# Optimization experiments

Measured on AMD Instinct MI355X. Metric: run time of the kernel, lower is better.

The kernel has to match this reference:

```python
import jax, jax.numpy as jnp
import numpy as np

GRID_SIZE = 16
KH = KW = 3


def setup_inputs() -> dict:
    key = jax.random.key(0)
    k1, k2, k3, k4 = jax.random.split(key, 4)
    B, H, W, C, F = 8, 32, 32, 64, 64
    x = jax.random.normal(k1, (B, H, W, C), dtype=jnp.float32)
    control_points = jax.random.normal(k2, (F, C, KH, KW, GRID_SIZE), dtype=jnp.float32) * 0.1
    w1 = jax.random.normal(k3, (F, C, KH, KW), dtype=jnp.float32) * 0.1
    w2 = jax.random.normal(k4, (F, C, KH, KW), dtype=jnp.float32) * 0.1
    return {"x": x, "control_points": control_points, "w1": w1, "w2": w2}


def _extract_patches_same(x, kh, kw):
    # x: (B,H,W,C), stride 1, TF 'SAME' padding -> (B,H,W,kh,kw,C)
    B, H, W, C = x.shape
    ph, pw = kh - 1, kw - 1
    xp = jnp.pad(x, ((0, 0), (ph // 2, ph - ph // 2), (pw // 2, pw - pw // 2), (0, 0)))
    taps = [xp[:, i:i + H, j:j + W, :] for i in range(kh) for j in range(kw)]
    return jnp.stack(taps, axis=3).reshape(B, H, W, kh, kw, C)


def reference(x, control_points, w1, w2):
    F, C, kh, kw, G = control_points.shape
    grid = jnp.linspace(-1.0, 1.0, G)
    patches = _extract_patches_same(x, kh, kw)  # (B,H,W,kh,kw,C)
    # spline: searchsorted + clip + linear interp on the fixed uniform grid
    xc = jnp.clip(patches, -1.0, 1.0)
    idx = jnp.clip(jnp.searchsorted(grid, xc, side='left') - 1, 0, G - 2)
    frac = (xc - grid[idx]) / (grid[idx + 1] - grid[idx])  # (B,H,W,kh,kw,C)
    # two-nonzero linear basis over control points -> (B,H,W,kh,kw,C,G)
    basis = (jax.nn.one_hot(idx, G, dtype=x.dtype) * (1.0 - frac)[..., None]
             + jax.nn.one_hot(idx + 1, G, dtype=x.dtype) * frac[..., None])
    # fuse w1 into control points, contract taps+channels+grid in one einsum
    wcp = w1[..., None] * control_points  # (F,C,kh,kw,G)
    out = jnp.einsum('bpqijcg,fcijg->bpqf', basis, wcp)
    out = out + jnp.einsum('bpqijc,fcij->bpqf', jax.nn.silu(patches), w2)
    return out  # (B,H,W,F)
```

## Files before the change

kernel.cpp:

```cpp
#include <hip/hip_runtime.h>


typedef _Float16 v8h __attribute__((ext_vector_type(8)));
typedef float    v4f __attribute__((ext_vector_type(4)));

#define NSLOT8  81920
#define NOUT4   131072

__global__ __launch_bounds__(256) void prep_wsw(const float* __restrict__ cp,
                                                const float* __restrict__ w1,
                                                const float* __restrict__ w2,
                                                _Float16* __restrict__ wsw,
                                                float* __restrict__ out) {
    int tid = blockIdx.x * 256 + threadIdx.x;
    if (tid < NSLOT8) {
        int lane = tid & 63;
        int rest = tid >> 6;
        int nt   = rest & 3;
        int ks   = rest >> 2;
        int kb   = ks * 32 + ((lane >> 4) << 3);
        int f    = (nt << 4) + (lane & 15);
        int chunk = kb / 640;
        int klb   = kb - chunk * 640;
        v8h o;
        if (klb < 576) {
            int c  = (chunk << 2) + klb / 144;
            int rb = klb % 144;
            int ij = rb >> 4;
            float w = w1[f * 576 + c * 9 + ij];
            const v4f* cpp = (const v4f*)(cp + (size_t)f * 9216 + c * 144 + rb);
            v4f lo = cpp[0], hi = cpp[1];
#pragma unroll
            for (int j = 0; j < 4; ++j) {
            o[j]     = (_Float16)(w * lo[j]);
            o[j + 4] = (_Float16)(w * hi[j]);
            }
        } else {
            int i2 = klb - 576;
            int c  = (chunk << 2) + (i2 >> 4);
            if ((i2 & 15) == 0) {
#pragma unroll
                for (int j = 0; j < 8; ++j)
                    o[j] = (_Float16)w2[f * 576 + c * 9 + j];
            } else {
#pragma unroll
                for (int j = 0; j < 8; ++j) o[j] = (_Float16)0.f;
                o[0] = (_Float16)w2[f * 576 + c * 9 + 8];
            }
        }
        ((v8h*)wsw)[tid] = o;
    }
    if (tid < NOUT4) ((v4f*)out)[tid] = (v4f){0.f, 0.f, 0.f, 0.f};
}

__global__ __launch_bounds__(256, 3) void kan_mfma(const float* __restrict__ x,
                                                   const _Float16* __restrict__ wsw,
                                                   float* __restrict__ out) {
    __shared__ __align__(16) char smem[41472];
    _Float16* sb  = (_Float16*)smem;
    float*    red = (float*)smem;

    int blk   = blockIdx.x;
    int kh    = blk >> 8;
    int rowid = blk & 255;
    int b = rowid >> 5, p = rowid & 31;
    int t = threadIdx.x, wv = t >> 6, lane = t & 63;
    int m = lane & 15, kq = lane >> 4;

    const int chs[4] = {0, 6, 11, 16};
    int ch0 = chs[kh], ch1 = chs[kh + 1];

    const float* xb = x + (size_t)b * 65536;

    int xoff[2], sbb[2], silb[2];
    unsigned prevPack[2] = {0u, 0u};
#pragma unroll
    for (int it = 0; it < 2; ++it) {
        int e  = t + it * 256;
        int ec = e < 288 ? e : 0;
        int px = ec / 9;
        int ij = ec - px * 9;
        int di = ij / 3;
        int dj = ij - di * 3;
        int row = p + di - 1;
        int col = px + dj - 1;
        bool ok  = ((unsigned)row < 32u) && ((unsigned)col < 32u);
        xoff[it] = ok ? ((row * 32 + col) * 64) : -1;
        sbb[it]  = px * 648 + ij * 16;
        silb[it] = px * 648 + 576 + ij;
    }

    v4f z4 = (v4f){0.f, 0.f, 0.f, 0.f};

    v4f vbuf[2];
#pragma unroll
    for (int it = 0; it < 2; ++it)
        vbuf[it] = (xoff[it] >= 0) ? *(const v4f*)(xb + xoff[it] + ch0 * 4) : z4;

    for (int i4 = t; i4 < 2592; i4 += 256) ((v4f*)sb)[i4] = z4;

    v4f acc[2][4];
#pragma unroll
    for (int i = 0; i < 2; ++i)
#pragma unroll
        for (int n = 0; n < 4; ++n) acc[i][n] = z4;

    __syncthreads();

    for (int gch = ch0; gch < ch1; ++gch) {
#pragma unroll
        for (int it = 0; it < 2; ++it) {
            if (t + it * 256 < 288) {
                v4f xv = vbuf[it];
                unsigned pp = prevPack[it];
                unsigned np = 0;
                _Float16* rp = sb + sbb[it];
                _Float16* sp = sb + silb[it];
#pragma unroll
                for (int cl = 0; cl < 4; ++cl) {
                    float v  = xv[cl];
                    float xc = fminf(fmaxf(v, -1.f), 1.f);
                    float tt = (xc + 1.f) * 7.5f;
                    int idx  = (int)tt;
                    if (idx > 14) idx = 14;
                    float fr = tt - (float)idx;
                    float sv = v * __builtin_amdgcn_rcpf(1.f + __expf(-v));
                    _Float16* q = rp + cl * 144;
                    if (gch > ch0) {
                        int pi = (pp >> (cl * 8)) & 255;
                        q[pi]     = (_Float16)0.f;
                        q[pi + 1] = (_Float16)0.f;
                    }
                    q[idx]     = (_Float16)(1.f - fr);
                    q[idx + 1] = (_Float16)fr;
                    sp[cl * 16] = (_Float16)sv;
                    np |= (unsigned)idx << (cl * 8);
                }
                prevPack[it] = np;
            }
        }
        __syncthreads();
        if (gch + 1 < ch1) {
#pragma unroll
            for (int it = 0; it < 2; ++it)
                vbuf[it] = (xoff[it] >= 0)
                         ? *(const v4f*)(xb + xoff[it] + (gch + 1) * 4) : z4;
        }
        const _Float16* ap = sb + m * 648 + (wv * 5) * 32 + kq * 8;
        const v8h* bp = (const v8h*)wsw + ((size_t)gch * 20 + wv * 5) * 256 + lane;
        v8h a0c = *(const v8h*)ap;
        v8h a1c = *(const v8h*)(ap + 16 * 648);
        v8h b0c = bp[0], b1c = bp[64], b2c = bp[128], b3c = bp[192];
#pragma unroll
        for (int s = 0; s < 5; ++s) {
            v8h a0n, a1n, b0n, b1n, b2n, b3n;
            if (s < 4) {
                const _Float16* ap2 = ap + (s + 1) * 32;
                a0n = *(const v8h*)ap2;
                a1n = *(const v8h*)(ap2 + 16 * 648);
                const v8h* bp2 = bp + (s + 1) * 256;
                b0n = bp2[0];
                b1n = bp2[64];
                b2n = bp2[128];
                b3n = bp2[192];
            }
            acc[0][0] = __builtin_amdgcn_mfma_f32_16x16x32_f16(a0c, b0c, acc[0][0], 0, 0, 0);
            acc[0][1] = __builtin_amdgcn_mfma_f32_16x16x32_f16(a0c, b1c, acc[0][1], 0, 0, 0);
            acc[0][2] = __builtin_amdgcn_mfma_f32_16x16x32_f16(a0c, b2c, acc[0][2], 0, 0, 0);
            acc[0][3] = __builtin_amdgcn_mfma_f32_16x16x32_f16(a0c, b3c, acc[0][3], 0, 0, 0);
            acc[1][0] = __builtin_amdgcn_mfma_f32_16x16x32_f16(a1c, b0c, acc[1][0], 0, 0, 0);
            acc[1][1] = __builtin_amdgcn_mfma_f32_16x16x32_f16(a1c, b1c, acc[1][1], 0, 0, 0);
            acc[1][2] = __builtin_amdgcn_mfma_f32_16x16x32_f16(a1c, b2c, acc[1][2], 0, 0, 0);
            acc[1][3] = __builtin_amdgcn_mfma_f32_16x16x32_f16(a1c, b3c, acc[1][3], 0, 0, 0);
            if (s < 4) {
                a0c = a0n; a1c = a1n;
                b0c = b0n; b1c = b1n; b2c = b2n; b3c = b3n;
            }
        }
        __syncthreads();
    }

#pragma unroll
    for (int mt = 0; mt < 2; ++mt)
#pragma unroll
        for (int nt = 0; nt < 4; ++nt)
#pragma unroll
            for (int r = 0; r < 4; ++r)
                red[wv * 2080 + (mt * 16 + kq * 4 + r) * 65 + nt * 16 + m] = acc[mt][nt][r];
    __syncthreads();
    int f = t & 63, pxg = t >> 6;
    float* op = out + (size_t)rowid * 2048 + f;
#pragma unroll
    for (int i = 0; i < 8; ++i) {
        int px = pxg * 8 + i;
        float s = red[px * 65 + f] + red[2080 + px * 65 + f]
                + red[4160 + px * 65 + f] + red[6240 + px * 65 + f];
        atomicAdd(op + px * 64, s);
    }
}

extern "C" void kernel_launch(void* const* d_in, const int* in_sizes, int n_in,
                              void* d_out, int out_size, void* d_ws, size_t ws_size,
                              hipStream_t stream) {
    const float* x  = (const float*)d_in[0];
    const float* cp = (const float*)d_in[1];
    const float* w1 = (const float*)d_in[2];
    const float* w2 = (const float*)d_in[3];
    _Float16* wsw = (_Float16*)d_ws;
    float*    outp = (float*)d_out;

    prep_wsw<<<512, 256, 0, stream>>>(cp, w1, w2, wsw, outp);
    kan_mfma<<<768, 256, 0, stream>>>(x, wsw, outp);
}
```

Measured before the change: 87.84 us.

## Build spline and SiLU MFMA A-fragments in registers instead of via LDS

Each lane now builds its own A-operand fragment straight from global x. Spline fragments come from clamp/index math on one value per row, placing the two nonzero basis weights. SiLU fragments gather up to eight neighbouring taps. This removes the shared-memory basis buffer, its zero-fill and scatter stores, and the two barriers per channel group. In exchange it reloads x redundantly across lanes and waves, recomputes exp for SiLU taps, and drops the explicit software prefetch of A and B fragments.

```diff
diff --git a/kernel.cpp b/kernel.cpp
--- a/kernel.cpp
+++ b/kernel.cpp
@@ -3,6 +3,8 @@
 
 typedef _Float16 v8h __attribute__((ext_vector_type(8)));
 typedef float    v4f __attribute__((ext_vector_type(4)));
+typedef unsigned int u32;
+typedef u32      v4u __attribute__((ext_vector_type(4)));
 
 #define NSLOT8  81920
 #define NOUT4   131072
@@ -32,8 +34,8 @@
             v4f lo = cpp[0], hi = cpp[1];
 #pragma unroll
             for (int j = 0; j < 4; ++j) {
-            o[j]     = (_Float16)(w * lo[j]);
-            o[j + 4] = (_Float16)(w * hi[j]);
+                o[j]     = (_Float16)(w * lo[j]);
+                o[j + 4] = (_Float16)(w * hi[j]);
             }
         } else {
             int i2 = klb - 576;
@@ -53,12 +55,61 @@
     if (tid < NOUT4) ((v4f*)out)[tid] = (v4f){0.f, 0.f, 0.f, 0.f};
 }
 
+__device__ inline u32 h2u(float f) {
+    union { _Float16 h; unsigned short u; } c;
+    c.h = (_Float16)f;
+    return (u32)c.u;
+}
+
+__device__ inline v8h spline_frag(float v, int g0) {
+    float xc = fminf(fmaxf(v, -1.f), 1.f);
+    float tt = (xc + 1.f) * 7.5f;
+    int idx  = (int)tt;
+    if (idx > 14) idx = 14;
+    float fr = tt - (float)idx;
+    int r0 = idx - g0;
+    u32 lo = h2u(1.f - fr);
+    u32 hi = h2u(fr);
+    u32 pair = lo | (hi << 16);
+    int wq = r0 >> 1;
+    int ro = r0 & 1;
+    v4u w;
+#pragma unroll
+    for (int q = 0; q < 4; ++q) {
+        u32 val = (q == wq) ? (ro ? (lo << 16) : pair)
+                            : ((ro && q == wq + 1) ? hi : 0u);
+        w[q] = val;
+    }
+    union { v4u u; v8h h; } cvt;
+    cvt.u = w;
+    return cvt.h;
+}
+
+__device__ inline v8h silu_frag(const float* __restrict__ xb, int xc,
+                                int p, int pxq, int ijh) {
+    v8h a;
+#pragma unroll
+    for (int j = 0; j < 8; ++j) {
+        int ij = ijh + j;
+        float sv = 0.f;
+        if (ij < 9) {
+            int di = (ij * 11) >> 5;
+            int dj = ij - 3 * di;
+            int row = p + di - 1;
+            int col = pxq + dj - 1;
+            float xv = ((unsigned)row < 32u && (unsigned)col < 32u)
+                     ? xb[(row * 32 + col) * 64 + xc] : 0.f;
+            sv = xv * __builtin_amdgcn_rcpf(1.f + __expf(-xv));
+        }
+        a[j] = (_Float16)sv;
+    }
+    return a;
+}
+
 __global__ __launch_bounds__(256, 3) void kan_mfma(const float* __restrict__ x,
                                                    const _Float16* __restrict__ wsw,
                                                    float* __restrict__ out) {
-    __shared__ __align__(16) char smem[41472];
-    _Float16* sb  = (_Float16*)smem;
-    float*    red = (float*)smem;
+    __shared__ __align__(16) float red[8320];
 
     int blk   = blockIdx.x;
     int kh    = blk >> 8;
@@ -72,112 +123,70 @@
 
     const float* xb = x + (size_t)b * 65536;
 
-    int xoff[2], sbb[2], silb[2];
-    unsigned prevPack[2] = {0u, 0u};
-#pragma unroll
-    for (int it = 0; it < 2; ++it) {
-        int e  = t + it * 256;
-        int ec = e < 288 ? e : 0;
-        int px = ec / 9;
-        int ij = ec - px * 9;
-        int di = ij / 3;
-        int dj = ij - di * 3;
-        int row = p + di - 1;
-        int col = px + dj - 1;
-        bool ok  = ((unsigned)row < 32u) && ((unsigned)col < 32u);
-        xoff[it] = ok ? ((row * 32 + col) * 64) : -1;
-        sbb[it]  = px * 648 + ij * 16;
-        silb[it] = px * 648 + 576 + ij;
+    int offA[5], offB[5], g0s[5];
+#pragma unroll
+    for (int s = 0; s < 5; ++s) {
+        int kst = wv * 5 + s;
+        int kk  = kst * 32 + kq * 8;
+        if (kk < 576) {
+            int cl = kk / 144;
+            int rr = kk - cl * 144;
+            int ij = rr >> 4;
+            g0s[s] = rr & 15;
+            int di = (ij * 11) >> 5;
+            int dj = ij - 3 * di;
+            int row = p + di - 1;
+            int c0  = m + dj - 1;
+            int c1  = c0 + 16;
+            bool okr = (unsigned)row < 32u;
+            offA[s] = (okr && (unsigned)c0 < 32u) ? (row * 32 + c0) * 64 + cl : -1;
+            offB[s] = (okr && (unsigned)c1 < 32u) ? (row * 32 + c1) * 64 + cl : -1;
+        } else {
+            g0s[s] = -(kk - 576) - 1;
+            offA[s] = 0;
+            offB[s] = 0;
+        }
     }
 
     v4f z4 = (v4f){0.f, 0.f, 0.f, 0.f};
-
-    v4f vbuf[2];
-#pragma unroll
-    for (int it = 0; it < 2; ++it)
-        vbuf[it] = (xoff[it] >= 0) ? *(const v4f*)(xb + xoff[it] + ch0 * 4) : z4;
-
-    for (int i4 = t; i4 < 2592; i4 += 256) ((v4f*)sb)[i4] = z4;
-
     v4f acc[2][4];
 #pragma unroll
     for (int i = 0; i < 2; ++i)
 #pragma unroll
         for (int n = 0; n < 4; ++n) acc[i][n] = z4;
 
-    __syncthreads();
-
     for (int gch = ch0; gch < ch1; ++gch) {
-#pragma unroll
-        for (int it = 0; it < 2; ++it) {
-            if (t + it * 256 < 288) {
-                v4f xv = vbuf[it];
-                unsigned pp = prevPack[it];
-                unsigned np = 0;
-                _Float16* rp = sb + sbb[it];
-                _Float16* sp = sb + silb[it];
-#pragma unroll
-                for (int cl = 0; cl < 4; ++cl) {
-                    float v  = xv[cl];
-                    float xc = fminf(fmaxf(v, -1.f), 1.f);
-                    float tt = (xc + 1.f) * 7.5f;
-                    int idx  = (int)tt;
-                    if (idx > 14) idx = 14;
-                    float fr = tt - (float)idx;
-                    float sv = v * __builtin_amdgcn_rcpf(1.f + __expf(-v));
-                    _Float16* q = rp + cl * 144;
-                    if (gch > ch0) {
-                        int pi = (pp >> (cl * 8)) & 255;
-                        q[pi]     = (_Float16)0.f;
-                        q[pi + 1] = (_Float16)0.f;
-                    }
-                    q[idx]     = (_Float16)(1.f - fr);
-                    q[idx + 1] = (_Float16)fr;
-                    sp[cl * 16] = (_Float16)sv;
-                    np |= (unsigned)idx << (cl * 8);
-                }
-                prevPack[it] = np;
+        const v8h* bp = (const v8h*)wsw + ((size_t)gch * 20 + wv * 5) * 256 + lane;
+        int xc4 = gch * 4;
+#pragma unroll
+        for (int s = 0; s < 5; ++s) {
+            v8h a0, a1;
+            int g0 = g0s[s];
+            if (g0 >= 0) {
+                float x0 = (offA[s] >= 0) ? xb[offA[s] + xc4] : 0.f;
+                float x1 = (offB[s] >= 0) ? xb[offB[s] + xc4] : 0.f;
+                a0 = spline_frag(x0, g0);
+                a1 = spline_frag(x1, g0);
+            } else {
+                int i2  = -1 - g0;
+                int cl  = i2 >> 4;
+                int ijh = i2 & 15;
+                a0 = silu_frag(xb, xc4 + cl, p, m, ijh);
+                a1 = silu_frag(xb, xc4 + cl, p, m + 16, ijh);
             }
-        }
-        __syncthreads();
-        if (gch + 1 < ch1) {
-#pragma unroll
-            for (int it = 0; it < 2; ++it)
-                vbuf[it] = (xoff[it] >= 0)
-                         ? *(const v4f*)(xb + xoff[it] + (gch + 1) * 4) : z4;
-        }
-        const _Float16* ap = sb + m * 648 + (wv * 5) * 32 + kq * 8;
-        const v8h* bp = (const v8h*)wsw + ((size_t)gch * 20 + wv * 5) * 256 + lane;
-        v8h a0c = *(const v8h*)ap;
-        v8h a1c = *(const v8h*)(ap + 16 * 648);
-        v8h b0c = bp[0], b1c = bp[64], b2c = bp[128], b3c = bp[192];
-#pragma unroll
-        for (int s = 0; s < 5; ++s) {
-            v8h a0n, a1n, b0n, b1n, b2n, b3n;
-            if (s < 4) {
-                const _Float16* ap2 = ap + (s + 1) * 32;
-                a0n = *(const v8h*)ap2;
-                a1n = *(const v8h*)(ap2 + 16 * 648);
-                const v8h* bp2 = bp + (s + 1) * 256;
-                b0n = bp2[0];
-                b1n = bp2[64];
-                b2n = bp2[128];
-                b3n = bp2[192];
-            }
-            acc[0][0] = __builtin_amdgcn_mfma_f32_16x16x32_f16(a0c, b0c, acc[0][0], 0, 0, 0);
-            acc[0][1] = __builtin_amdgcn_mfma_f32_16x16x32_f16(a0c, b1c, acc[0][1], 0, 0, 0);
-            acc[0][2] = __builtin_amdgcn_mfma_f32_16x16x32_f16(a0c, b2c, acc[0][2], 0, 0, 0);
-            acc[0][3] = __builtin_amdgcn_mfma_f32_16x16x32_f16(a0c, b3c, acc[0][3], 0, 0, 0);
-            acc[1][0] = __builtin_amdgcn_mfma_f32_16x16x32_f16(a1c, b0c, acc[1][0], 0, 0, 0);
-            acc[1][1] = __builtin_amdgcn_mfma_f32_16x16x32_f16(a1c, b1c, acc[1][1], 0, 0, 0);
-            acc[1][2] = __builtin_amdgcn_mfma_f32_16x16x32_f16(a1c, b2c, acc[1][2], 0, 0, 0);
-            acc[1][3] = __builtin_amdgcn_mfma_f32_16x16x32_f16(a1c, b3c, acc[1][3], 0, 0, 0);
-            if (s < 4) {
-                a0c = a0n; a1c = a1n;
-                b0c = b0n; b1c = b1n; b2c = b2n; b3c = b3n;
-            }
-        }
-        __syncthreads();
+            v8h b0 = bp[s * 256];
+            v8h b1 = bp[s * 256 + 64];
+            v8h b2 = bp[s * 256 + 128];
+            v8h b3 = bp[s * 256 + 192];
+            acc[0][0] = __builtin_amdgcn_mfma_f32_16x16x32_f16(a0, b0, acc[0][0], 0, 0, 0);
+            acc[0][1] = __builtin_amdgcn_mfma_f32_16x16x32_f16(a0, b1, acc[0][1], 0, 0, 0);
+            acc[0][2] = __builtin_amdgcn_mfma_f32_16x16x32_f16(a0, b2, acc[0][2], 0, 0, 0);
+            acc[0][3] = __builtin_amdgcn_mfma_f32_16x16x32_f16(a0, b3, acc[0][3], 0, 0, 0);
+            acc[1][0] = __builtin_amdgcn_mfma_f32_16x16x32_f16(a1, b0, acc[1][0], 0, 0, 0);
+            acc[1][1] = __builtin_amdgcn_mfma_f32_16x16x32_f16(a1, b1, acc[1][1], 0, 0, 0);
+            acc[1][2] = __builtin_amdgcn_mfma_f32_16x16x32_f16(a1, b2, acc[1][2], 0, 0, 0);
+            acc[1][3] = __builtin_amdgcn_mfma_f32_16x16x32_f16(a1, b3, acc[1][3], 0, 0, 0);
+        }
     }
 
 #pragma unroll
```

Result: slower. 130.2 us (+48.2%).

## Split rows into half-row blocks and double-buffer the LDS basis tiles

Applied to the files above, without the earlier changes.

Each block now covers 16 pixels (half a row) rather than 32, so the grid doubles to 1536 blocks and each wave holds one M-tile of accumulators. The LDS A-tile is double-buffered: the basis and SiLU values for the next channel group are scattered into the second buffer while MFMAs read the current one, which removes one barrier per iteration. The intent is more parallelism and overlap of scatter with matrix work. The cost is that every weight (B) fragment is now loaded from global memory twice as often relative to MFMA work, and the explicit register prefetch of operands was dropped.

```diff
diff --git a/kernel.cpp b/kernel.cpp
--- a/kernel.cpp
+++ b/kernel.cpp
@@ -6,6 +6,7 @@
 
 #define NSLOT8  81920
 #define NOUT4   131072
+#define BUFH    10368
 
 __global__ __launch_bounds__(256) void prep_wsw(const float* __restrict__ cp,
                                                 const float* __restrict__ w1,
@@ -32,8 +33,8 @@
             v4f lo = cpp[0], hi = cpp[1];
 #pragma unroll
             for (int j = 0; j < 4; ++j) {
-            o[j]     = (_Float16)(w * lo[j]);
-            o[j + 4] = (_Float16)(w * hi[j]);
+                o[j]     = (_Float16)(w * lo[j]);
+                o[j + 4] = (_Float16)(w * hi[j]);
             }
         } else {
             int i2 = klb - 576;
@@ -53,6 +54,36 @@
     if (tid < NOUT4) ((v4f*)out)[tid] = (v4f){0.f, 0.f, 0.f, 0.f};
 }
 
+__device__ inline void scatter4(v4f xv, _Float16* __restrict__ base,
+                                int sbb, int silb, unsigned& pk, bool doClear,
+                                bool active) {
+    if (!active) return;
+    _Float16* rp = base + sbb;
+    _Float16* sp = base + silb;
+    unsigned pp = pk, np = 0;
+#pragma unroll
+    for (int cl = 0; cl < 4; ++cl) {
+        float v  = xv[cl];
+        float xc = fminf(fmaxf(v, -1.f), 1.f);
+        float tt = (xc + 1.f) * 7.5f;
+        int idx  = (int)tt;
+        if (idx > 14) idx = 14;
+        float fr = tt - (float)idx;
+        float sv = v * __builtin_amdgcn_rcpf(1.f + __expf(-v));
+        _Float16* q = rp + cl * 144;
+        if (doClear) {
+            int pi = (pp >> (cl * 8)) & 255;
+            q[pi]     = (_Float16)0.f;
+            q[pi + 1] = (_Float16)0.f;
+        }
+        q[idx]     = (_Float16)(1.f - fr);
+        q[idx + 1] = (_Float16)fr;
+        sp[cl * 16] = (_Float16)sv;
+        np |= (unsigned)idx << (cl * 8);
+    }
+    pk = np;
+}
+
 __global__ __launch_bounds__(256, 3) void kan_mfma(const float* __restrict__ x,
                                                    const _Float16* __restrict__ wsw,
                                                    float* __restrict__ out) {
@@ -60,10 +91,10 @@
     _Float16* sb  = (_Float16*)smem;
     float*    red = (float*)smem;
 
-    int blk   = blockIdx.x;
-    int kh    = blk >> 8;
-    int rowid = blk & 255;
-    int b = rowid >> 5, p = rowid & 31;
+    int blk = blockIdx.x;
+    int kh  = blk >> 9;
+    int id  = blk & 511;
+    int b = id >> 6, p = (id >> 1) & 31, half = id & 1;
     int t = threadIdx.x, wv = t >> 6, lane = t & 63;
     int m = lane & 15, kq = lane >> 4;
 
@@ -72,129 +103,79 @@
 
     const float* xb = x + (size_t)b * 65536;
 
-    int xoff[2], sbb[2], silb[2];
-    unsigned prevPack[2] = {0u, 0u};
-#pragma unroll
-    for (int it = 0; it < 2; ++it) {
-        int e  = t + it * 256;
-        int ec = e < 288 ? e : 0;
-        int px = ec / 9;
-        int ij = ec - px * 9;
-        int di = ij / 3;
-        int dj = ij - di * 3;
+    bool active = t < 144;
+    int xoff, sbb, silb;
+    {
+        int e   = active ? t : 0;
+        int q16 = e / 9;
+        int ij  = e - q16 * 9;
+        int di  = ij / 3;
+        int dj  = ij - di * 3;
         int row = p + di - 1;
-        int col = px + dj - 1;
-        bool ok  = ((unsigned)row < 32u) && ((unsigned)col < 32u);
-        xoff[it] = ok ? ((row * 32 + col) * 64) : -1;
-        sbb[it]  = px * 648 + ij * 16;
-        silb[it] = px * 648 + 576 + ij;
+        int col = half * 16 + q16 + dj - 1;
+        bool ok = ((unsigned)row < 32u) && ((unsigned)col < 32u) && active;
+        xoff = ok ? (row * 32 + col) * 64 : -1;
+        sbb  = q16 * 648 + ij * 16;
+        silb = q16 * 648 + 576 + ij;
     }
 
     v4f z4 = (v4f){0.f, 0.f, 0.f, 0.f};
-
-    v4f vbuf[2];
+    v4f acc[4];
 #pragma unroll
-    for (int it = 0; it < 2; ++it)
-        vbuf[it] = (xoff[it] >= 0) ? *(const v4f*)(xb + xoff[it] + ch0 * 4) : z4;
+    for (int n = 0; n < 4; ++n) acc[n] = z4;
 
     for (int i4 = t; i4 < 2592; i4 += 256) ((v4f*)sb)[i4] = z4;
 
-    v4f acc[2][4];
-#pragma unroll
-    for (int i = 0; i < 2; ++i)
-#pragma unroll
-        for (int n = 0; n < 4; ++n) acc[i][n] = z4;
+    v4f vbuf = (xoff >= 0) ? *(const v4f*)(xb + xoff + ch0 * 4) : z4;
+    unsigned pk0 = 0u, pk1 = 0u;
 
     __syncthreads();
 
-    for (int gch = ch0; gch < ch1; ++gch) {
-#pragma unroll
-        for (int it = 0; it < 2; ++it) {
-            if (t + it * 256 < 288) {
-                v4f xv = vbuf[it];
-                unsigned pp = prevPack[it];
-                unsigned np = 0;
-                _Float16* rp = sb + sbb[it];
-                _Float16* sp = sb + silb[it];
-#pragma unroll
-                for (int cl = 0; cl < 4; ++cl) {
-                    float v  = xv[cl];
-                    float xc = fminf(fmaxf(v, -1.f), 1.f);
-                    float tt = (xc + 1.f) * 7.5f;
-                    int idx  = (int)tt;
-                    if (idx > 14) idx = 14;
-                    float fr = tt - (float)idx;
-                    float sv = v * __builtin_amdgcn_rcpf(1.f + __expf(-v));
-                    _Float16* q = rp + cl * 144;
-                    if (gch > ch0) {
-                        int pi = (pp >> (cl * 8)) & 255;
-                        q[pi]     = (_Float16)0.f;
-                        q[pi + 1] = (_Float16)0.f;
-                    }
-                    q[idx]     = (_Float16)(1.f - fr);
-                    q[idx + 1] = (_Float16)fr;
-                    sp[cl * 16] = (_Float16)sv;
-                    np |= (unsigned)idx << (cl * 8);
-                }
-                prevPack[it] = np;
-            }
+    scatter4(vbuf, sb, sbb, silb, pk0, false, active);
+    if (ch0 + 1 < ch1)
+        vbuf = (xoff >= 0) ? *(const v4f*)(xb + xoff + (ch0 + 1) * 4) : z4;
+    __syncthreads();
+
+    for (int g = ch0; g < ch1; ++g) {
+        int cur = (g - ch0) & 1;
+        if (g + 1 < ch1) {
+            if (cur == 0)
+                scatter4(vbuf, sb + BUFH, sbb, silb, pk1, g > ch0, active);
+            else
+                scatter4(vbuf, sb, sbb, silb, pk0, g > ch0, active);
+            if (g + 2 < ch1)
+                vbuf = (xoff >= 0) ? *(const v4f*)(xb + xoff + (g + 2) * 4) : z4;
         }
-        __syncthreads();
-        if (gch + 1 < ch1) {
-#pragma unroll
-            for (int it = 0; it < 2; ++it)
-                vbuf[it] = (xoff[it] >= 0)
-                         ? *(const v4f*)(xb + xoff[it] + (gch + 1) * 4) : z4;
-        }
-        const _Float16* ap = sb + m * 648 + (wv * 5) * 32 + kq * 8;
-        const v8h* bp = (const v8h*)wsw + ((size_t)gch * 20 + wv * 5) * 256 + lane;
-        v8h a0c = *(const v8h*)ap;
-        v8h a1c = *(const v8h*)(ap + 16 * 648);
-        v8h b0c = bp[0], b1c = bp[64], b2c = bp[128], b3c = bp[192];
+        const _Float16* ap = sb + cur * BUFH + m * 648 + (wv * 5) * 32 + kq * 8;
+        const v8h* bp = (const v8h*)wsw + ((size_t)g * 20 + wv * 5) * 256 + lane;
 #pragma unroll
         for (int s = 0; s < 5; ++s) {
-            v8h a0n, a1n, b0n, b1n, b2n, b3n;
-            if (s < 4) {
-                const _Float16* ap2 = ap + (s + 1) * 32;
-                a0n = *(const v8h*)ap2;
-                a1n = *(const v8h*)(ap2 + 16 * 648);
-                const v8h* bp2 = bp + (s + 1) * 256;
-                b0n = bp2[0];
-                b1n = bp2[64];
-                b2n = bp2[128];
-                b3n = bp2[192];
-            }
-            acc[0][0] = __builtin_amdgcn_mfma_f32_16x16x32_f16(a0c, b0c, acc[0][0], 0, 0, 0);
-            acc[0][1] = __builtin_amdgcn_mfma_f32_16x16x32_f16(a0c, b1c, acc[0][1], 0, 0, 0);
-            acc[0][2] = __builtin_amdgcn_mfma_f32_16x16x32_f16(a0c, b2c, acc[0][2], 0, 0, 0);
-            acc[0][3] = __builtin_amdgcn_mfma_f32_16x16x32_f16(a0c, b3c, acc[0][3], 0, 0, 0);
-            acc[1][0] = __builtin_amdgcn_mfma_f32_16x16x32_f16(a1c, b0c, acc[1][0], 0, 0, 0);
-            acc[1][1] = __builtin_amdgcn_mfma_f32_16x16x32_f16(a1c, b1c, acc[1][1], 0, 0, 0);
-            acc[1][2] = __builtin_amdgcn_mfma_f32_16x16x32_f16(a1c, b2c, acc[1][2], 0, 0, 0);
-            acc[1][3] = __builtin_amdgcn_mfma_f32_16x16x32_f16(a1c, b3c, acc[1][3], 0, 0, 0);
-            if (s < 4) {
-                a0c = a0n; a1c = a1n;
-                b0c = b0n; b1c = b1n; b2c = b2n; b3c = b3n;
-            }
+            v8h a  = *(const v8h*)(ap + s * 32);
+            v8h b0 = bp[s * 256];
+            v8h b1 = bp[s * 256 + 64];
+            v8h b2 = bp[s * 256 + 128];
+            v8h b3 = bp[s * 256 + 192];
+            acc[0] = __builtin_amdgcn_mfma_f32_16x16x32_f16(a, b0, acc[0], 0, 0, 0);
+            acc[1] = __builtin_amdgcn_mfma_f32_16x16x32_f16(a, b1, acc[1], 0, 0, 0);
+            acc[2] = __builtin_amdgcn_mfma_f32_16x16x32_f16(a, b2, acc[2], 0, 0, 0);
+            acc[3] = __builtin_amdgcn_mfma_f32_16x16x32_f16(a, b3, acc[3], 0, 0, 0);
         }
         __syncthreads();
     }
 
 #pragma unroll
-    for (int mt = 0; mt < 2; ++mt)
+    for (int nt = 0; nt < 4; ++nt)
 #pragma unroll
-        for (int nt = 0; nt < 4; ++nt)
-#pragma unroll
-            for (int r = 0; r < 4; ++r)
-                red[wv * 2080 + (mt * 16 + kq * 4 + r) * 65 + nt * 16 + m] = acc[mt][nt][r];
+        for (int r = 0; r < 4; ++r)
+            red[wv * 1040 + (kq * 4 + r) * 65 + nt * 16 + m] = acc[nt][r];
     __syncthreads();
     int f = t & 63, pxg = t >> 6;
-    float* op = out + (size_t)rowid * 2048 + f;
+    float* op = out + ((size_t)(b * 32 + p) * 32 + half * 16) * 64 + f;
 #pragma unroll
-    for (int i = 0; i < 8; ++i) {
-        int px = pxg * 8 + i;
-        float s = red[px * 65 + f] + red[2080 + px * 65 + f]
-                + red[4160 + px * 65 + f] + red[6240 + px * 65 + f];
+    for (int i = 0; i < 4; ++i) {
+        int px = pxg * 4 + i;
+        float s = red[px * 65 + f] + red[1040 + px * 65 + f]
+                + red[2080 + px * 65 + f] + red[3120 + px * 65 + f];
         atomicAdd(op + px * 64, s);
     }
 }
@@ -210,5 +191,5 @@
     float*    outp = (float*)d_out;
 
     prep_wsw<<<512, 256, 0, stream>>>(cp, w1, w2, wsw, outp);
-    kan_mfma<<<768, 256, 0, stream>>>(x, wsw, outp);
+    kan_mfma<<<1536, 256, 0, stream>>>(x, wsw, outp);
 }
```

Measured after the change: 96.36 us. 9.7% more time.

## Swizzle LDS operand layout, split channels into four even chunks, raise occupancy

Applied to the files above, without the earlier changes.

The LDS A-operand tile changes from a padded 648-half row stride to an unpadded 1280-byte row with an XOR swizzle, so the MFMA fragment reads and the scattered basis writes avoid bank conflicts with less shared memory. The channel-group split changes from uneven 6/5/5 chunks to four even chunks of 4, and the grid grows from 768 to 1024 blocks, which adds more atomic partial sums. The launch bound is raised to 4 blocks per SM, and the manual software prefetch of A/B fragments is removed in favour of direct loads, which may expose load latency.

```diff
diff --git a/kernel.cpp b/kernel.cpp
--- a/kernel.cpp
+++ b/kernel.cpp
@@ -32,8 +32,8 @@
             v4f lo = cpp[0], hi = cpp[1];
 #pragma unroll
             for (int j = 0; j < 4; ++j) {
-            o[j]     = (_Float16)(w * lo[j]);
-            o[j + 4] = (_Float16)(w * hi[j]);
+                o[j]     = (_Float16)(w * lo[j]);
+                o[j + 4] = (_Float16)(w * hi[j]);
             }
         } else {
             int i2 = klb - 576;
@@ -53,12 +53,11 @@
     if (tid < NOUT4) ((v4f*)out)[tid] = (v4f){0.f, 0.f, 0.f, 0.f};
 }
 
-__global__ __launch_bounds__(256, 3) void kan_mfma(const float* __restrict__ x,
+__global__ __launch_bounds__(256, 4) void kan_mfma(const float* __restrict__ x,
                                                    const _Float16* __restrict__ wsw,
                                                    float* __restrict__ out) {
-    __shared__ __align__(16) char smem[41472];
-    _Float16* sb  = (_Float16*)smem;
-    float*    red = (float*)smem;
+    __shared__ __align__(16) char smem[40960];
+    float* red = (float*)smem;
 
     int blk   = blockIdx.x;
     int kh    = blk >> 8;
@@ -67,55 +66,55 @@
     int t = threadIdx.x, wv = t >> 6, lane = t & 63;
     int m = lane & 15, kq = lane >> 4;
 
-    const int chs[4] = {0, 6, 11, 16};
-    int ch0 = chs[kh], ch1 = chs[kh + 1];
-
+    int ch0 = kh * 4, ch1 = ch0 + 4;
     const float* xb = x + (size_t)b * 65536;
 
-    int xoff[2], sbb[2], silb[2];
-    unsigned prevPack[2] = {0u, 0u};
+    int xoff[2], sbase[2], smask[2], ijb[2];
+    bool act[2];
 #pragma unroll
     for (int it = 0; it < 2; ++it) {
-        int e  = t + it * 256;
-        int ec = e < 288 ? e : 0;
-        int px = ec / 9;
-        int ij = ec - px * 9;
+        bool a = (it == 0) || (lane < 8);
+        int e  = a ? (wv * 72 + it * 64 + lane) : 0;
+        int q  = e / 9;
+        int ij = e - q * 9;
         int di = ij / 3;
         int dj = ij - di * 3;
         int row = p + di - 1;
-        int col = px + dj - 1;
-        bool ok  = ((unsigned)row < 32u) && ((unsigned)col < 32u);
-        xoff[it] = ok ? ((row * 32 + col) * 64) : -1;
-        sbb[it]  = px * 648 + ij * 16;
-        silb[it] = px * 648 + 576 + ij;
+        int col = q + dj - 1;
+        bool ok = ((unsigned)row < 32u) && ((unsigned)col < 32u) && a;
+        act[it]   = a;
+        xoff[it]  = ok ? (row * 32 + col) * 64 : -1;
+        sbase[it] = q * 1280;
+        smask[it] = (q & 7) << 4;
+        ijb[it]   = ij * 32;
     }
 
     v4f z4 = (v4f){0.f, 0.f, 0.f, 0.f};
+    v4f acc[2][4];
+#pragma unroll
+    for (int i = 0; i < 2; ++i)
+#pragma unroll
+        for (int n = 0; n < 4; ++n) acc[i][n] = z4;
+
+    for (int i4 = t; i4 < 2560; i4 += 256) ((v4f*)smem)[i4] = z4;
 
     v4f vbuf[2];
 #pragma unroll
     for (int it = 0; it < 2; ++it)
         vbuf[it] = (xoff[it] >= 0) ? *(const v4f*)(xb + xoff[it] + ch0 * 4) : z4;
-
-    for (int i4 = t; i4 < 2592; i4 += 256) ((v4f*)sb)[i4] = z4;
-
-    v4f acc[2][4];
-#pragma unroll
-    for (int i = 0; i < 2; ++i)
-#pragma unroll
-        for (int n = 0; n < 4; ++n) acc[i][n] = z4;
+    unsigned pk[2] = {0u, 0u};
 
     __syncthreads();
 
     for (int gch = ch0; gch < ch1; ++gch) {
 #pragma unroll
         for (int it = 0; it < 2; ++it) {
-            if (t + it * 256 < 288) {
+            if (act[it]) {
                 v4f xv = vbuf[it];
-                unsigned pp = prevPack[it];
-                unsigned np = 0;
-                _Float16* rp = sb + sbb[it];
-                _Float16* sp = sb + silb[it];
+                char* rowp = smem + sbase[it];
+                int mask = smask[it];
+                int jb   = ijb[it];
+                unsigned pp = pk[it], np = 0;
 #pragma unroll
                 for (int cl = 0; cl < 4; ++cl) {
                     float v  = xv[cl];
@@ -125,18 +124,20 @@
                     if (idx > 14) idx = 14;
                     float fr = tt - (float)idx;
                     float sv = v * __builtin_amdgcn_rcpf(1.f + __expf(-v));
-                    _Float16* q = rp + cl * 144;
+                    int sb0 = cl * 288 + jb;
                     if (gch > ch0) {
-                        int pi = (pp >> (cl * 8)) & 255;
-                        q[pi]     = (_Float16)0.f;
-                        q[pi + 1] = (_Float16)0.f;
+                        int pb = sb0 + (int)((pp >> (cl * 8)) & 255) * 2;
+                        *(_Float16*)(rowp + (pb ^ mask))       = (_Float16)0.f;
+                        *(_Float16*)(rowp + ((pb + 2) ^ mask)) = (_Float16)0.f;
                     }
-                    q[idx]     = (_Float16)(1.f - fr);
-                    q[idx + 1] = (_Float16)fr;
-                    sp[cl * 16] = (_Float16)sv;
+                    int wb = sb0 + idx * 2;
+                    *(_Float16*)(rowp + (wb ^ mask))       = (_Float16)(1.f - fr);
+                    *(_Float16*)(rowp + ((wb + 2) ^ mask)) = (_Float16)fr;
+                    *(_Float16*)(rowp + ((1152 + cl * 32 + (jb >> 4)) ^ mask))
+                        = (_Float16)sv;
                     np |= (unsigned)idx << (cl * 8);
                 }
-                prevPack[it] = np;
+                pk[it] = np;
             }
         }
         __syncthreads();
@@ -146,36 +147,26 @@
                 vbuf[it] = (xoff[it] >= 0)
                          ? *(const v4f*)(xb + xoff[it] + (gch + 1) * 4) : z4;
         }
-        const _Float16* ap = sb + m * 648 + (wv * 5) * 32 + kq * 8;
         const v8h* bp = (const v8h*)wsw + ((size_t)gch * 20 + wv * 5) * 256 + lane;
-        v8h a0c = *(const v8h*)ap;
-        v8h a1c = *(const v8h*)(ap + 16 * 648);
-        v8h b0c = bp[0], b1c = bp[64], b2c = bp[128], b3c = bp[192];
+        int mbase = m * 1280;
+        int mm    = (m & 7) << 4;
 #pragma unroll
         for (int s = 0; s < 5; ++s) {
-            v8h a0n, a1n, b0n, b1n, b2n, b3n;
-            if (s < 4) {
-                const _Float16* ap2 = ap + (s + 1) * 32;
-                a0n = *(const v8h*)ap2;
-                a1n = *(const v8h*)(ap2 + 16 * 648);
-                const v8h* bp2 = bp + (s + 1) * 256;
-                b0n = bp2[0];
-                b1n = bp2[64];
-                b2n = bp2[128];
-                b3n = bp2[192];
-            }
-            acc[0][0] = __builtin_amdgcn_mfma_f32_16x16x32_f16(a0c, b0c, acc[0][0], 0, 0, 0);
-            acc[0][1] = __builtin_amdgcn_mfma_f32_16x16x32_f16(a0c, b1c, acc[0][1], 0, 0, 0);
-            acc[0][2] = __builtin_amdgcn_mfma_f32_16x16x32_f16(a0c, b2c, acc[0][2], 0, 0, 0);
-            acc[0][3] = __builtin_amdgcn_mfma_f32_16x16x32_f16(a0c, b3c, acc[0][3], 0, 0, 0);
-            acc[1][0] = __builtin_amdgcn_mfma_f32_16x16x32_f16(a1c, b0c, acc[1][0], 0, 0, 0);
-            acc[1][1] = __builtin_amdgcn_mfma_f32_16x16x32_f16(a1c, b1c, acc[1][1], 0, 0, 0);
-            acc[1][2] = __builtin_amdgcn_mfma_f32_16x16x32_f16(a1c, b2c, acc[1][2], 0, 0, 0);
-            acc[1][3] = __builtin_amdgcn_mfma_f32_16x16x32_f16(a1c, b3c, acc[1][3], 0, 0, 0);
-            if (s < 4) {
-                a0c = a0n; a1c = a1n;
-                b0c = b0n; b1c = b1n; b2c = b2n; b3c = b3n;
-            }
+            int kx = (((wv * 5 + s) * 64) + (kq * 16)) ^ mm;
+            v8h a0 = *(const v8h*)(smem + mbase + kx);
+            v8h a1 = *(const v8h*)(smem + mbase + 20480 + kx);
+            v8h b0 = bp[s * 256];
+            v8h b1 = bp[s * 256 + 64];
+            v8h b2 = bp[s * 256 + 128];
+            v8h b3 = bp[s * 256 + 192];
+            acc[0][0] = __builtin_amdgcn_mfma_f32_16x16x32_f16(a0, b0, acc[0][0], 0, 0, 0);
+            acc[0][1] = __builtin_amdgcn_mfma_f32_16x16x32_f16(a0, b1, acc[0][1], 0, 0, 0);
+            acc[0][2] = __builtin_amdgcn_mfma_f32_16x16x32_f16(a0, b2, acc[0][2], 0, 0, 0);
+            acc[0][3] = __builtin_amdgcn_mfma_f32_16x16x32_f16(a0, b3, acc[0][3], 0, 0, 0);
+            acc[1][0] = __builtin_amdgcn_mfma_f32_16x16x32_f16(a1, b0, acc[1][0], 0, 0, 0);
+            acc[1][1] = __builtin_amdgcn_mfma_f32_16x16x32_f16(a1, b1, acc[1][1], 0, 0, 0);
+            acc[1][2] = __builtin_amdgcn_mfma_f32_16x16x32_f16(a1, b2, acc[1][2], 0, 0, 0);
+            acc[1][3] = __builtin_amdgcn_mfma_f32_16x16x32_f16(a1, b3, acc[1][3], 0, 0, 0);
         }
         __syncthreads();
     }
@@ -210,5 +201,5 @@
     float*    outp = (float*)d_out;
 
     prep_wsw<<<512, 256, 0, stream>>>(cp, w1, w2, wsw, outp);
-    kan_mfma<<<768, 256, 0, stream>>>(x, wsw, outp);
+    kan_mfma<<<1024, 256, 0, stream>>>(x, wsw, outp);
 }
```

New measurement: 83.00 us. 1.06x faster.
